# Optimization experiments

Hardware: AMD Instinct MI355X
Metric: run time of the kernel (lower is better)

## Reference

```python
import jax, jax.numpy as jnp
import numpy as np

D_MODEL = 1024
NUM_HEADS = 16
HEAD_DIM = D_MODEL // NUM_HEADS
SCALE = HEAD_DIM ** -0.5


def setup_inputs() -> dict:
    key = jax.random.key(0)
    ks = jax.random.split(key, 9)
    s = 1.0 / np.sqrt(D_MODEL)
    return {
        "query": jax.random.normal(ks[0], (4, 2048, D_MODEL), dtype=jnp.float32),
        "Wq": jax.random.normal(ks[1], (D_MODEL, D_MODEL), dtype=jnp.float32) * s,
        "bq": jax.random.normal(ks[2], (D_MODEL,), dtype=jnp.float32) * 0.01,
        "Wk": jax.random.normal(ks[3], (D_MODEL, D_MODEL), dtype=jnp.float32) * s,
        "bk": jax.random.normal(ks[4], (D_MODEL,), dtype=jnp.float32) * 0.01,
        "Wv": jax.random.normal(ks[5], (D_MODEL, D_MODEL), dtype=jnp.float32) * s,
        "bv": jax.random.normal(ks[6], (D_MODEL,), dtype=jnp.float32) * 0.01,
        "Wo": jax.random.normal(ks[7], (D_MODEL, D_MODEL), dtype=jnp.float32) * s,
        "bo": jax.random.normal(ks[8], (D_MODEL,), dtype=jnp.float32) * 0.01,
    }


def reference(query, Wq, bq, Wk, bk, Wv, bv, Wo, bo):
    # Self-attention (key=value=query). dropout=0, no mask, so chunked
    # computation equals full softmax attention exactly.
    b, s, d = query.shape
    q = (query @ Wq + bq).reshape(b, s, NUM_HEADS, HEAD_DIM)
    k = (query @ Wk + bk).reshape(b, s, NUM_HEADS, HEAD_DIM)
    v = (query @ Wv + bv).reshape(b, s, NUM_HEADS, HEAD_DIM)
    # scores: [b, h, s_q, s_k]
    scores = jnp.einsum("bqhd,bkhd->bhqk", q, k) * SCALE
    attn = jax.nn.softmax(scores, axis=-1)
    ctx = jnp.einsum("bhqk,bkhd->bqhd", attn, v).reshape(b, s, d)
    return ctx @ Wo + bo
```

## Files before the change

### kernel.cpp

```cpp
#include <hip/hip_runtime.h>
#include <stdint.h>

#define NHEADS 16
#define HDIM   64
#define SEQ    2048
#define BATCH  4
#define DM     1024
#define MTOT   (BATCH*SEQ)
#define SCALE  0.125f
#define QSCALE 0.18033688011112042f

typedef unsigned short u16;
typedef __attribute__((ext_vector_type(8))) short short8;
typedef __attribute__((ext_vector_type(4))) float f32x4;
typedef __attribute__((ext_vector_type(16))) float f32x16;
typedef __attribute__((ext_vector_type(4))) unsigned int u32x4;

__device__ __forceinline__ u16 f2bf(float f) {
  uint32_t u = __builtin_bit_cast(uint32_t, f);
  u += 0x7FFFu + ((u >> 16) & 1u);
  return (u16)(u >> 16);
}

__device__ __forceinline__ float fexp2(float x) {
#if __has_builtin(__builtin_amdgcn_exp2f)
  return __builtin_amdgcn_exp2f(x);
#else
  float r; asm("v_exp_f32 %0, %1\n\ts_nop 1" : "=v"(r) : "v"(x)); return r;
#endif
}

__device__ __forceinline__ f32x4 mfma16(short8 a, short8 b, f32x4 c) {
  return __builtin_amdgcn_mfma_f32_16x16x32_bf16(a, b, c, 0, 0, 0);
}
__device__ __forceinline__ f32x16 mfma32(short8 a, short8 b, f32x16 c) {
  return __builtin_amdgcn_mfma_f32_32x32x16_bf16(a, b, c, 0, 0, 0);
}

__device__ __forceinline__ void gload16(const u16* g, u16* l) {
  __builtin_amdgcn_global_load_lds((const __attribute__((address_space(1))) void*)g,
                                   (__attribute__((address_space(3))) void*)l,
                                   16, 0, 0);
}

#define LDSP(base, row, boff) \
  ((u16*)((char*)(base) + (((row) << 7) + ((boff) ^ (((row) & 7) << 4)))))

__global__ __launch_bounds__(256) void k_conv(const float* __restrict__ in, u16* __restrict__ out) {
  size_t i = (size_t)blockIdx.x * 256 + threadIdx.x;
  const float4* p = (const float4*)(in + i * 8);
  float4 a = p[0], b = p[1];
  u16 r[8] = {f2bf(a.x), f2bf(a.y), f2bf(a.z), f2bf(a.w),
              f2bf(b.x), f2bf(b.y), f2bf(b.z), f2bf(b.w)};
  *(short8*)(out + i * 8) = *(const short8*)r;
}

__global__ __launch_bounds__(256) void k_convw(const float* __restrict__ w0, const float* __restrict__ w1,
                                               const float* __restrict__ w2, const float* __restrict__ w3,
                                               u16* __restrict__ o0, u16* __restrict__ o1,
                                               u16* __restrict__ o2, u16* __restrict__ o3) {
  const float* W = blockIdx.z==0?w0: blockIdx.z==1?w1: blockIdx.z==2?w2:w3;
  u16* O        = blockIdx.z==0?o0: blockIdx.z==1?o1: blockIdx.z==2?o2:o3;
  __shared__ float tile[32][33];
  int t = threadIdx.x;
  int k0 = blockIdx.y*32, n0 = blockIdx.x*32;
  int r = t >> 5, c = t & 31;
  #pragma unroll
  for (int p = 0; p < 4; ++p) tile[r + 8*p][c] = W[(size_t)(k0 + r + 8*p)*DM + n0 + c];
  __syncthreads();
  #pragma unroll
  for (int p = 0; p < 4; ++p) O[(size_t)(n0 + r + 8*p)*DM + k0 + c] = f2bf(tile[c][r + 8*p]);
}

template<int MODE>
__global__ __launch_bounds__(256) void k_gemm(
    const u16* __restrict__ A,
    const u16* __restrict__ WtQ, const u16* __restrict__ WtK, const u16* __restrict__ WtV,
    const float* __restrict__ bQ, const float* __restrict__ bK, const float* __restrict__ bV,
    u16* __restrict__ oQ, u16* __restrict__ oK, u16* __restrict__ oV,
    float* __restrict__ oF)
{
  __shared__ u16 As[128*32];
  __shared__ u16 Bs[128*32];
  const int t = threadIdx.x;
  const int lane = t & 63;
  const int lo = lane & 15, q4 = lane >> 4;
  const int w  = t >> 6, wm = w >> 1, wn = w & 1;

  int m0, n0, z;
  if (MODE == 0) {
    int L = blockIdx.x + 8 * blockIdx.y + 512 * blockIdx.z;
    int work = (L & 7) * 192 + (L >> 3);
    z  = work % 3;
    n0 = ((work / 3) & 7) * 128;
    m0 = (work / 24) * 128;
  } else {
    int L = blockIdx.x + 8 * blockIdx.y;
    int work = (L & 7) * 64 + (L >> 3);
    z  = 0;
    n0 = (work & 7) * 128;
    m0 = (work >> 3) * 128;
  }

  const u16* Wt; const float* bias;
  if (MODE == 0) {
    Wt   = (z==0)?WtQ:(z==1)?WtK:WtV;
    bias = (z==0)?bQ:(z==1)?bK:bV;
  } else { Wt = WtQ; bias = bQ; }

  f32x4 acc[4][4] = {};

  const int gr = lane >> 2;
  const int gc = (lane & 3) * 8;

  for (int kt = 0; kt < 32; ++kt) {
    const int k0 = kt * 32;
    __syncthreads();
    gload16(A  + (size_t)(m0 + w*32 +  0 + gr)*DM + k0 + gc, As + (w*32 +  0)*32);
    gload16(A  + (size_t)(m0 + w*32 + 16 + gr)*DM + k0 + gc, As + (w*32 + 16)*32);
    gload16(Wt + (size_t)(n0 + w*32 +  0 + gr)*DM + k0 + gc, Bs + (w*32 +  0)*32);
    gload16(Wt + (size_t)(n0 + w*32 + 16 + gr)*DM + k0 + gc, Bs + (w*32 + 16)*32);
    __syncthreads();

    short8 af[4], bf[4];
    #pragma unroll
    for (int i = 0; i < 4; ++i)
      af[i] = *(const short8*)(As + (wm*64 + i*16 + lo)*32 + q4*8);
    #pragma unroll
    for (int i = 0; i < 4; ++i)
      bf[i] = *(const short8*)(Bs + (wn*64 + i*16 + lo)*32 + q4*8);
    #pragma unroll
    for (int i = 0; i < 4; ++i)
      #pragma unroll
      for (int j = 0; j < 4; ++j)
        acc[i][j] = mfma16(af[i], bf[j], acc[i][j]);
  }

  #pragma unroll
  for (int i = 0; i < 4; ++i) {
    #pragma unroll
    for (int j = 0; j < 4; ++j) {
      int col = n0 + wn*64 + j*16 + lo;
      float bvv = bias[col];
      #pragma unroll
      for (int r = 0; r < 4; ++r) {
        int row = m0 + wm*64 + i*16 + q4*4 + r;
        float v = acc[i][j][r] + bvv;
        if (MODE == 0) {
          int b = row >> 11, s = row & 2047, h = col >> 6, d = col & 63;
          if (z == 2) oV[(size_t)((b*16 + h)*64 + d)*SEQ + s] = f2bf(v);
          else if (z == 0) oQ[(size_t)((b*16 + h)*SEQ + s)*HDIM + d] = f2bf(v * QSCALE);
          else             oK[(size_t)((b*16 + h)*SEQ + s)*HDIM + d] = f2bf(v);
        } else {
          oF[(size_t)row*DM + col] = v;
        }
      }
    }
  }
}

__global__ __launch_bounds__(512, 4) void k_attn(
    const u16* __restrict__ Q,
    const u16* __restrict__ K,
    const u16* __restrict__ VT,
    u16* __restrict__ O)
{
  __shared__ u16 lds[16384];
  const int t = threadIdx.x, lane = t & 63, w = t >> 6;
  const int l31 = lane & 31, h = lane >> 5;
  const int bh = blockIdx.x, qt = blockIdx.y;
  const int qw = qt*256 + w*32;

  const u16* Qp = Q  + ((size_t)bh * SEQ + qw) * HDIM;
  const u16* Kp = K  + (size_t)bh * SEQ * HDIM;
  const u16* Vp = VT + (size_t)bh * HDIM * SEQ;

  short8 qf[4];
  #pragma unroll
  for (int c = 0; c < 4; ++c)
    qf[c] = *(const short8*)(Qp + (size_t)l31*HDIM + c*16 + h*8);

  f32x16 acc[2] = {};
  float l_run = 0.f;

  const int sr = t >> 3, sc = t & 7;
  const u16* Kg = Kp + (size_t)sr * HDIM;
  const u16* Vg = Vp + (size_t)sr * SEQ;

  short8 kr = *(const short8*)(Kg + sc*8);
  short8 vr = *(const short8*)(Vg + sc*8);
  *(short8*)LDSP(lds,        sr, sc*16) = kr;
  *(short8*)LDSP(lds + 4096, sr, sc*16) = vr;
  kr = *(const short8*)(Kg + (size_t)64*HDIM + sc*8);
  vr = *(const short8*)(Vg + 64 + sc*8);
  __syncthreads();

  for (int kt = 0; kt < 32; ++kt) {
    u16* Ksc = lds + (size_t)(kt & 1) * 8192;
    u16* Vsc = Ksc + 4096;
    if (kt + 1 < 32) {
      u16* Ksn = lds + (size_t)((kt + 1) & 1) * 8192;
      *(short8*)LDSP(Ksn,        sr, sc*16) = kr;
      *(short8*)LDSP(Ksn + 4096, sr, sc*16) = vr;
      int kn = (kt + 2 < 32 ? kt + 2 : 31) * 64;
      kr = *(const short8*)(Kg + (size_t)kn*HDIM + sc*8);
      vr = *(const short8*)(Vg + kn + sc*8);
    }

    #pragma unroll
    for (int kb = 0; kb < 2; ++kb) {
      short8 kf[4];
      #pragma unroll
      for (int c = 0; c < 4; ++c)
        kf[c] = *(const short8*)LDSP(Ksc, kb*32 + l31, c*32 + h*16);

      f32x16 s = {};
      #pragma unroll
      for (int c = 0; c < 4; ++c) s = mfma32(kf[c], qf[c], s);

      float sum = 0.f;
      uint32_t W[8];
      #pragma unroll
      for (int i8 = 0; i8 < 8; ++i8) {
        float pe = fexp2(s[2*i8]);
        float po = fexp2(s[2*i8+1]);
        sum += pe + po;
        W[i8] = __builtin_amdgcn_perm(__builtin_bit_cast(uint32_t, po),
                                      __builtin_bit_cast(uint32_t, pe),
                                      0x07060302u);
      }
      l_run += sum;

      #pragma unroll
      for (int k2 = 0; k2 < 2; ++k2) {
        auto r0 = __builtin_amdgcn_permlane32_swap(W[4*k2 + 0], W[4*k2 + 2], false, false);
        auto r1 = __builtin_amdgcn_permlane32_swap(W[4*k2 + 1], W[4*k2 + 3], false, false);
        u32x4 pw; pw[0] = r0[0]; pw[1] = r1[0]; pw[2] = r0[1]; pw[3] = r1[1];
        short8 pf = __builtin_bit_cast(short8, pw);
        #pragma unroll
        for (int dt = 0; dt < 2; ++dt) {
          short8 vf = *(const short8*)LDSP(Vsc, dt*32 + l31, kb*64 + k2*32 + h*16);
          acc[dt] = mfma32(vf, pf, acc[dt]);
        }
      }
    }
    __syncthreads();
  }

  u16* ep = lds + w*2048;
  float lt = l_run + __shfl_xor(l_run, 32);
  float inv = 1.f / lt;
  #pragma unroll
  for (int dt = 0; dt < 2; ++dt)
    #pragma unroll
    for (int grp = 0; grp < 4; ++grp) {
      int dbase = dt*32 + 8*grp + 4*h;
      uint32_t w0 = __builtin_amdgcn_perm(
          __builtin_bit_cast(uint32_t, acc[dt][grp*4+1] * inv),
          __builtin_bit_cast(uint32_t, acc[dt][grp*4+0] * inv), 0x07060302u);
      uint32_t w1 = __builtin_amdgcn_perm(
          __builtin_bit_cast(uint32_t, acc[dt][grp*4+3] * inv),
          __builtin_bit_cast(uint32_t, acc[dt][grp*4+2] * inv), 0x07060302u);
      uint2 pk; pk.x = w0; pk.y = w1;
      *(uint2*)LDSP(ep, l31, 2*dbase) = pk;
    }
  const int b = bh >> 4, hh = bh & 15;
  #pragma unroll
  for (int it = 0; it < 4; ++it) {
    int row = it*8 + (lane >> 3);
    int s = qw + row;
    short8 v = *(const short8*)LDSP(ep, row, (lane & 7)*16);
    *(short8*)(O + ((size_t)(b*SEQ + s)*NHEADS + hh)*HDIM + (lane & 7)*8) = v;
  }
}

extern "C" void kernel_launch(void* const* d_in, const int* in_sizes, int n_in,
                              void* d_out, int out_size, void* d_ws, size_t ws_size,
                              hipStream_t stream) {
  const float* query = (const float*)d_in[0];
  const float* Wq = (const float*)d_in[1]; const float* bq = (const float*)d_in[2];
  const float* Wk = (const float*)d_in[3]; const float* bk = (const float*)d_in[4];
  const float* Wv = (const float*)d_in[5]; const float* bv = (const float*)d_in[6];
  const float* Wo = (const float*)d_in[7]; const float* bo = (const float*)d_in[8];
  float* out = (float*)d_out;

  u16* qb  = (u16*)d_ws;
  u16* wt0 = qb  + (size_t)MTOT*DM;
  u16* wt1 = wt0 + (size_t)DM*DM;
  u16* wt2 = wt1 + (size_t)DM*DM;
  u16* wt3 = wt2 + (size_t)DM*DM;
  u16* qp  = wt3 + (size_t)DM*DM;
  u16* kp  = qp  + (size_t)MTOT*DM;
  u16* vt  = kp  + (size_t)MTOT*DM;

  k_conv<<<dim3(MTOT*DM/8/256), 256, 0, stream>>>(query, qb);
  k_convw<<<dim3(32, 32, 4), 256, 0, stream>>>(Wq, Wk, Wv, Wo, wt0, wt1, wt2, wt3);
  k_gemm<0><<<dim3(8, 64, 3), 256, 0, stream>>>(qb, wt0, wt1, wt2, bq, bk, bv, qp, kp, vt, nullptr);
  k_attn<<<dim3(64, 8), 512, 0, stream>>>(qp, kp, vt, qb );
  k_gemm<1><<<dim3(8, 64, 1), 256, 0, stream>>>(qb, wt3, nullptr, nullptr, bo, nullptr, nullptr,
                                                nullptr, nullptr, nullptr, out);
}
```

Before: 288.2 us.

## Rewrite projection GEMMs as 256x256 double-buffered 8-wave pipelined kernel

Replaces the 128x128, 4-wave, single-buffered GEMM with a 256x256-tile, 512-thread kernel. It uses a 64-wide K step, XOR-swizzled LDS, double-buffered global_load_lds staging interleaved with MFMA phases, setprio and explicit vmcnt waits. QKV becomes one launch over a concatenated 3072-wide weight, which relies on wt0..wt2 being contiguous, and the grid is XCD-aware. The goal is more data reuse and overlap of loads with compute. The cost is 128KB of LDS per block and lower occupancy. The tail tile is clamped and redundantly reloaded.

New measurement: 299.4 us. 1.04x slower.

```diff
diff --git a/kernel.cpp b/kernel.cpp
--- a/kernel.cpp
+++ b/kernel.cpp
@@ -45,6 +45,12 @@
 
 #define LDSP(base, row, boff) \
   ((u16*)((char*)(base) + (((row) << 7) + ((boff) ^ (((row) & 7) << 4)))))
+
+__device__ __forceinline__ void hardbar() {
+  __builtin_amdgcn_sched_barrier(0);
+  __builtin_amdgcn_s_barrier();
+  __builtin_amdgcn_sched_barrier(0);
+}
 
 __global__ __launch_bounds__(256) void k_conv(const float* __restrict__ in, u16* __restrict__ out) {
   size_t i = (size_t)blockIdx.x * 256 + threadIdx.x;
@@ -73,82 +79,105 @@
 }
 
 template<int MODE>
-__global__ __launch_bounds__(256) void k_gemm(
-    const u16* __restrict__ A,
-    const u16* __restrict__ WtQ, const u16* __restrict__ WtK, const u16* __restrict__ WtV,
+__global__ __launch_bounds__(512, 2) void k_gemm8(
+    const u16* __restrict__ A, const u16* __restrict__ Wt,
     const float* __restrict__ bQ, const float* __restrict__ bK, const float* __restrict__ bV,
     u16* __restrict__ oQ, u16* __restrict__ oK, u16* __restrict__ oV,
     float* __restrict__ oF)
 {
-  __shared__ u16 As[128*32];
-  __shared__ u16 Bs[128*32];
-  const int t = threadIdx.x;
-  const int lane = t & 63;
-  const int lo = lane & 15, q4 = lane >> 4;
-  const int w  = t >> 6, wm = w >> 1, wn = w & 1;
-
-  int m0, n0, z;
-  if (MODE == 0) {
-    int L = blockIdx.x + 8 * blockIdx.y + 512 * blockIdx.z;
-    int work = (L & 7) * 192 + (L >> 3);
-    z  = work % 3;
-    n0 = ((work / 3) & 7) * 128;
-    m0 = (work / 24) * 128;
-  } else {
-    int L = blockIdx.x + 8 * blockIdx.y;
-    int work = (L & 7) * 64 + (L >> 3);
-    z  = 0;
-    n0 = (work & 7) * 128;
-    m0 = (work >> 3) * 128;
-  }
-
-  const u16* Wt; const float* bias;
-  if (MODE == 0) {
-    Wt   = (z==0)?WtQ:(z==1)?WtK:WtV;
-    bias = (z==0)?bQ:(z==1)?bK:bV;
-  } else { Wt = WtQ; bias = bQ; }
-
-  f32x4 acc[4][4] = {};
-
-  const int gr = lane >> 2;
-  const int gc = (lane & 3) * 8;
-
-  for (int kt = 0; kt < 32; ++kt) {
-    const int k0 = kt * 32;
-    __syncthreads();
-    gload16(A  + (size_t)(m0 + w*32 +  0 + gr)*DM + k0 + gc, As + (w*32 +  0)*32);
-    gload16(A  + (size_t)(m0 + w*32 + 16 + gr)*DM + k0 + gc, As + (w*32 + 16)*32);
-    gload16(Wt + (size_t)(n0 + w*32 +  0 + gr)*DM + k0 + gc, Bs + (w*32 +  0)*32);
-    gload16(Wt + (size_t)(n0 + w*32 + 16 + gr)*DM + k0 + gc, Bs + (w*32 + 16)*32);
-    __syncthreads();
-
-    short8 af[4], bf[4];
-    #pragma unroll
-    for (int i = 0; i < 4; ++i)
-      af[i] = *(const short8*)(As + (wm*64 + i*16 + lo)*32 + q4*8);
-    #pragma unroll
-    for (int i = 0; i < 4; ++i)
-      bf[i] = *(const short8*)(Bs + (wn*64 + i*16 + lo)*32 + q4*8);
-    #pragma unroll
-    for (int i = 0; i < 4; ++i)
-      #pragma unroll
-      for (int j = 0; j < 4; ++j)
-        acc[i][j] = mfma16(af[i], bf[j], acc[i][j]);
-  }
-
-  #pragma unroll
-  for (int i = 0; i < 4; ++i) {
+  __shared__ u16 lds[65536];
+  u16* const A0 = lds;
+  u16* const B0 = lds + 16384;
+  u16* const A1 = lds + 32768;
+  u16* const B1 = lds + 49152;
+  const int t = threadIdx.x, lane = t & 63, w = t >> 6;
+  const int wm = w >> 2, wn = w & 3;
+  const int lo = lane & 15, ksl = lane >> 4;
+
+  int m0, n0;
+  { int L = blockIdx.x, xcd = L & 7, idx = L >> 3;
+    if (MODE == 0) { m0 = (xcd*4 + idx/12)*256; n0 = (idx%12)*256; }
+    else           { m0 = (xcd*4 + idx/4 )*256; n0 = (idx%4 )*256; }
+  }
+
+  const int srow = w*8 + (lane>>3);
+  const int sgof = ((lane & 7) ^ ((lane >> 3) & 7)) * 8;
+
+  f32x4 acc[8][4] = {};
+  short8 bfr[4][2];
+
+  auto ST = [&](const u16* S, int rc0, u16* LB, int rowbase, int tile) {
+    int tS = tile < 16 ? tile : 15;
+    gload16(S + (size_t)(rc0 + rowbase + srow)*DM + tS*64 + sgof,
+            LB + (rowbase + w*8)*64);
+  };
+  auto LDX = [&](u16* base, int row, int slot) -> short8 {
+    return *(const short8*)(base + row*64 + ((slot ^ (row & 7)) * 8));
+  };
+
+#define STAGEH(S, RC, LB, H, TILE) { ST(S, RC, LB, (H)*128, TILE); ST(S, RC, LB, (H)*128 + 64, TILE); }
+
+#define GPH(Q, AB, BB, DOB, SS, SRC0, SLB, SH, STILE, DOVM)                        \
+  {                                                                                \
+    if (DOB) {                                                                     \
+      _Pragma("unroll") for (int j = 0; j < 4; ++j) {                              \
+        bfr[j][0] = LDX(BB, wn*64 + j*16 + lo, ksl);                               \
+        bfr[j][1] = LDX(BB, wn*64 + j*16 + lo, 4 + ksl);                           \
+      }                                                                            \
+    }                                                                              \
+    short8 af[2][2];                                                               \
+    _Pragma("unroll") for (int ri = 0; ri < 2; ++ri) {                             \
+      af[ri][0] = LDX(AB, wm*128 + ((Q)*2 + ri)*16 + lo, ksl);                     \
+      af[ri][1] = LDX(AB, wm*128 + ((Q)*2 + ri)*16 + lo, 4 + ksl);                 \
+    }                                                                              \
+    STAGEH(SS, SRC0, SLB, SH, STILE);                                              \
+    __builtin_amdgcn_s_setprio(1);                                                 \
+    _Pragma("unroll") for (int ri = 0; ri < 2; ++ri)                               \
+      _Pragma("unroll") for (int j = 0; j < 4; ++j)                                \
+        _Pragma("unroll") for (int ks = 0; ks < 2; ++ks)                           \
+          acc[(Q)*2 + ri][j] = mfma16(af[ri][ks], bfr[j][ks], acc[(Q)*2 + ri][j]); \
+    __builtin_amdgcn_s_setprio(0);                                                 \
+    if (DOVM) { asm volatile("s_waitcnt vmcnt(4)" ::: "memory"); }                 \
+    hardbar();                                                                     \
+  }
+
+  STAGEH(A,  m0, A0, 0, 0); STAGEH(A,  m0, A0, 1, 0);
+  STAGEH(Wt, n0, B0, 0, 0); STAGEH(Wt, n0, B0, 1, 0);
+  STAGEH(Wt, n0, B1, 0, 1); STAGEH(Wt, n0, B1, 1, 1);
+  asm volatile("s_waitcnt vmcnt(4)" ::: "memory");
+  hardbar();
+
+  for (int i = 0; i < 8; ++i) {
+    const int t1 = 2*i + 1, t2 = 2*i + 2, t3 = 2*i + 3;
+    GPH(0, A0, B0, 1, A,  m0, A1, 0, t1, 0)
+    GPH(1, A0, B0, 0, A,  m0, A1, 1, t1, 0)
+    GPH(2, A0, B0, 0, Wt, n0, B0, 0, t2, 0)
+    GPH(3, A0, B0, 0, Wt, n0, B0, 1, t2, 1)
+    GPH(0, A1, B1, 1, A,  m0, A0, 0, t2, 0)
+    GPH(1, A1, B1, 0, A,  m0, A0, 1, t2, 0)
+    GPH(2, A1, B1, 0, Wt, n0, B1, 0, t3, 0)
+    GPH(3, A1, B1, 0, Wt, n0, B1, 1, t3, 1)
+  }
+  asm volatile("s_waitcnt vmcnt(0)" ::: "memory");
+
+#undef GPH
+#undef STAGEH
+
+  const int z = (MODE == 0) ? (n0 >> 10) : 0;
+  const float* bias = (MODE == 0) ? ((z==0) ? bQ : (z==1) ? bK : bV) : bQ;
+  #pragma unroll
+  for (int ii = 0; ii < 8; ++ii) {
     #pragma unroll
     for (int j = 0; j < 4; ++j) {
       int col = n0 + wn*64 + j*16 + lo;
-      float bvv = bias[col];
+      float bvv = bias[(MODE == 0) ? (col & 1023) : col];
       #pragma unroll
       for (int r = 0; r < 4; ++r) {
-        int row = m0 + wm*64 + i*16 + q4*4 + r;
-        float v = acc[i][j][r] + bvv;
+        int row = m0 + wm*128 + ii*16 + ksl*4 + r;
+        float v = acc[ii][j][r] + bvv;
         if (MODE == 0) {
-          int b = row >> 11, s = row & 2047, h = col >> 6, d = col & 63;
-          if (z == 2) oV[(size_t)((b*16 + h)*64 + d)*SEQ + s] = f2bf(v);
+          int b = row >> 11, s = row & 2047, h = (col >> 6) & 15, d = col & 63;
+          if (z == 2)      oV[(size_t)((b*16 + h)*64 + d)*SEQ + s] = f2bf(v);
           else if (z == 0) oQ[(size_t)((b*16 + h)*SEQ + s)*HDIM + d] = f2bf(v * QSCALE);
           else             oK[(size_t)((b*16 + h)*SEQ + s)*HDIM + d] = f2bf(v);
         } else {
@@ -295,8 +324,8 @@
 
   k_conv<<<dim3(MTOT*DM/8/256), 256, 0, stream>>>(query, qb);
   k_convw<<<dim3(32, 32, 4), 256, 0, stream>>>(Wq, Wk, Wv, Wo, wt0, wt1, wt2, wt3);
-  k_gemm<0><<<dim3(8, 64, 3), 256, 0, stream>>>(qb, wt0, wt1, wt2, bq, bk, bv, qp, kp, vt, nullptr);
+  k_gemm8<0><<<dim3(384), 512, 0, stream>>>(qb, wt0, bq, bk, bv, qp, kp, vt, nullptr);
   k_attn<<<dim3(64, 8), 512, 0, stream>>>(qp, kp, vt, qb );
-  k_gemm<1><<<dim3(8, 64, 1), 256, 0, stream>>>(qb, wt3, nullptr, nullptr, bo, nullptr, nullptr,
-                                                nullptr, nullptr, nullptr, out);
-}
+  k_gemm8<1><<<dim3(128), 512, 0, stream>>>(qb, wt3, bo, nullptr, nullptr,
+                                            nullptr, nullptr, nullptr, out);
+}
```
